# Optimization experiments

Measured on AMD Instinct MI355X. Metric: run time of the kernel, lower is better.

## Reference

```python
import jax, jax.numpy as jnp
import numpy as np

HIDDEN = 1024
N_HEADS = 16
HEAD_DIM = HIDDEN // N_HEADS


def apply_rope(x, freqs):
    # x: [b, s, h, d]; freqs: [s, d//2]
    b, s, h, d = x.shape
    x2 = x.reshape(b, s, h, d // 2, 2)
    x_real, x_imag = x2[..., 0], x2[..., 1]
    cos = jnp.cos(freqs)[None, :, None, :]  # [1, s, 1, d//2]
    sin = jnp.sin(freqs)[None, :, None, :]
    out_real = x_real * cos - x_imag * sin
    out_imag = x_real * sin + x_imag * cos
    return jnp.stack([out_real, out_imag], axis=-1).reshape(b, s, h, d)


def setup_inputs() -> dict:
    key = jax.random.key(0)
    k_x, k_f, k_wq, k_bq, k_wo, k_bo = jax.random.split(key, 6)
    b, s = 2, 2048
    x = jax.random.normal(k_x, (b, s, HIDDEN), dtype=jnp.float32)
    freqs = jax.random.normal(k_f, (s, HEAD_DIM // 2), dtype=jnp.float32)
    lim = 1.0 / np.sqrt(HIDDEN)
    W_qkv = jax.random.uniform(k_wq, (HIDDEN, 3 * HIDDEN), jnp.float32, -lim, lim)
    b_qkv = jax.random.uniform(k_bq, (3 * HIDDEN,), jnp.float32, -lim, lim)
    W_out = jax.random.uniform(k_wo, (HIDDEN, HIDDEN), jnp.float32, -lim, lim)
    b_out = jax.random.uniform(k_bo, (HIDDEN,), jnp.float32, -lim, lim)
    return {"x": x, "freqs": freqs, "W_qkv": W_qkv, "b_qkv": b_qkv,
            "W_out": W_out, "b_out": b_out}


def reference(x, freqs, W_qkv, b_qkv, W_out, b_out):
    b, s, c = x.shape
    h, d = N_HEADS, HEAD_DIM
    qkv = jnp.einsum('bsc,cf->bsf', x, W_qkv) + b_qkv  # [b, s, 3*c]
    qkv = qkv.reshape(b, s, 3, h, d)
    q, k, v = qkv[:, :, 0], qkv[:, :, 1], qkv[:, :, 2]  # [b, s, h, d]
    q = apply_rope(q, freqs)
    k = apply_rope(k, freqs)
    scale = 1.0 / np.sqrt(d).astype(np.float32)
    scores = jnp.einsum('bqhd,bkhd->bhqk', q, k) * scale  # [b, h, s, s]
    attn = jax.nn.softmax(scores, axis=-1)
    out = jnp.einsum('bhqk,bkhd->bqhd', attn, v).reshape(b, s, c)
    return jnp.einsum('bsc,cf->bsf', out, W_out) + b_out
```

## Files before the change

### kernel.cpp

```cpp
#include <hip/hip_runtime.h>
#include <math.h>

constexpr int kB = 2;
constexpr int kS = 2048;
constexpr int kC = 1024;
constexpr int kH = 16;
constexpr int kD = 64;
constexpr int kF = 3072;
constexpr int kT = kB * kS;

typedef __attribute__((ext_vector_type(8))) short short8v;
typedef __attribute__((ext_vector_type(4))) short short4v;
typedef __attribute__((ext_vector_type(4))) float f32x4;
typedef __attribute__((ext_vector_type(16))) float f32x16;

__device__ __forceinline__ short f2bf(float f) {
    unsigned u = __builtin_bit_cast(unsigned, f);
    u += 0x7fffu + ((u >> 16) & 1u);
    return (short)(u >> 16);
}

__device__ __forceinline__ unsigned cvtpk(float a, float b) {
    unsigned r;
    asm("v_cvt_pk_bf16_f32 %0, %1, %2" : "=v"(r) : "v"(a), "v"(b));
    return r;
}

__device__ __forceinline__ unsigned pk_bf16(float a, float b) {
    unsigned ua = __builtin_bit_cast(unsigned, a);
    ua += 0x7fffu + ((ua >> 16) & 1u);
    unsigned ub = __builtin_bit_cast(unsigned, b);
    ub += 0x7fffu + ((ub >> 16) & 1u);
    return (ua >> 16) | (ub & 0xffff0000u);
}

__device__ __forceinline__ void gl_lds16(const void* g, void* l) {
    __builtin_amdgcn_global_load_lds(
        (const __attribute__((address_space(1))) char*)g,
        (__attribute__((address_space(3))) char*)l, 16, 0, 0);
}

__device__ __forceinline__ f32x4 mfma16(short8v a, short8v b, f32x4 c) {
    return __builtin_amdgcn_mfma_f32_16x16x32_bf16(a, b, c, 0, 0, 0);
}
__device__ __forceinline__ f32x16 mfma32(short8v a, short8v b, f32x16 c) {
    return __builtin_amdgcn_mfma_f32_32x32x16_bf16(a, b, c, 0, 0, 0);
}

__device__ __forceinline__ void tcvt_body(const float* __restrict__ w,
                                          short* __restrict__ wt, int K, int N,
                                          int bx, int by, int t, float Ts[64][65]) {
    const int n0 = bx * 64, k0 = by * 64;
    const int r = t >> 4, c4 = (t & 15) * 4;
#pragma unroll
    for (int rr = 0; rr < 64; rr += 16) {
        float4 v = *reinterpret_cast<const float4*>(&w[(size_t)(k0 + r + rr) * N + n0 + c4]);
        Ts[r + rr][c4 + 0] = v.x; Ts[r + rr][c4 + 1] = v.y;
        Ts[r + rr][c4 + 2] = v.z; Ts[r + rr][c4 + 3] = v.w;
    }
    __syncthreads();
#pragma unroll
    for (int rr = 0; rr < 64; rr += 16) {
        int n = r + rr;
        short4v o = { f2bf(Ts[c4 + 0][n]), f2bf(Ts[c4 + 1][n]),
                      f2bf(Ts[c4 + 2][n]), f2bf(Ts[c4 + 3][n]) };
        *reinterpret_cast<short4v*>(&wt[(size_t)(n0 + n) * K + k0 + c4]) = o;
    }
}

__global__ __launch_bounds__(256) void prep_kernel(
    const float* __restrict__ x, short* __restrict__ xb,
    const float* __restrict__ wq, short* __restrict__ wqt,
    const float* __restrict__ wo, short* __restrict__ wot,
    const float* __restrict__ freqs, float* __restrict__ cost,
    float* __restrict__ sint) {
    __shared__ float Ts[64][65];
    const int bid = blockIdx.x, t = threadIdx.x;
    if (bid < 4096) {
        int i = bid * 256 + t;
        float4 v = reinterpret_cast<const float4*>(x)[i];
        short4v o = { f2bf(v.x), f2bf(v.y), f2bf(v.z), f2bf(v.w) };
        reinterpret_cast<short4v*>(xb)[i] = o;
    } else if (bid < 4864) {
        int i = bid - 4096;
        tcvt_body(wq, wqt, kC, kF, i % 48, i / 48, t, Ts);
    } else if (bid < 5120) {
        int i = bid - 4864;
        tcvt_body(wo, wot, kC, kC, i % 16, i / 16, t, Ts);
    } else {
        int i = (bid - 5120) * 256 + t;
        float f = freqs[i];
        float s, c;
        sincosf(f, &s, &c);
        cost[i] = c; sint[i] = s;
    }
}

__device__ __forceinline__ void gemm_main(const short* __restrict__ A,
                                          const short* __restrict__ Bt,
                                          int m0, int n0, short* Als, short* Bls,
                                          f32x4 acc[4][4]) {
    const int tid = threadIdx.x, wid = tid >> 6, lane = tid & 63;
    const int srow = lane >> 3, schunk = lane & 7;
    const int fr = lane & 15, fg = lane >> 4;
    const int wm = (wid >> 1) * 64, wn = (wid & 1) * 64;
    for (int kt = 0; kt < 1024; kt += 64) {
        __syncthreads();
#pragma unroll
        for (int j = 0; j < 4; ++j) {
            int i = wid * 4 + j;
            int row = i * 8 + srow;
            gl_lds16(&A[(size_t)(m0 + row) * 1024 + kt + ((schunk ^ (row & 7)) << 3)],
                     &Als[i * 512]);
        }
#pragma unroll
        for (int j = 0; j < 4; ++j) {
            int i = wid * 4 + j;
            int row = i * 8 + srow;
            gl_lds16(&Bt[(size_t)(n0 + row) * 1024 + kt + ((schunk ^ (row & 7)) << 3)],
                     &Bls[i * 512]);
        }
        __syncthreads();
#pragma unroll
        for (int kk = 0; kk < 2; ++kk) {
            short8v af[4], bf[4];
#pragma unroll
            for (int fm = 0; fm < 4; ++fm) {
                int row = wm + fm * 16 + fr;
                af[fm] = *reinterpret_cast<const short8v*>(
                    &Als[row * 64 + (((fg + 4 * kk) ^ (row & 7)) << 3)]);
            }
#pragma unroll
            for (int fn = 0; fn < 4; ++fn) {
                int row = wn + fn * 16 + fr;
                bf[fn] = *reinterpret_cast<const short8v*>(
                    &Bls[row * 64 + (((fg + 4 * kk) ^ (row & 7)) << 3)]);
            }
#pragma unroll
            for (int fm = 0; fm < 4; ++fm)
#pragma unroll
                for (int fn = 0; fn < 4; ++fn)
                    acc[fm][fn] = mfma16(af[fm], bf[fn], acc[fm][fn]);
        }
    }
}

__global__ __launch_bounds__(256) void qkv_gemm_kernel(
    const short* __restrict__ xb, const short* __restrict__ wqt,
    const float* __restrict__ bias, const float* __restrict__ cost,
    const float* __restrict__ sint,
    short* __restrict__ qg, short* __restrict__ kg, short* __restrict__ vt) {
    __shared__ __attribute__((aligned(16))) short Als[128 * 64];
    __shared__ __attribute__((aligned(16))) short Bls[128 * 64];
    f32x4 acc[4][4] = {};
    const int tid = threadIdx.x, wid = tid >> 6, lane = tid & 63;
    const int m0 = blockIdx.y * 128, n0 = blockIdx.x * 128;
    gemm_main(xb, wqt, m0, n0, Als, Bls, acc);

    const int fr = lane & 15, fg = lane >> 4;
    const int wm = (wid >> 1) * 64, wn = (wid & 1) * 64;
    const int which = (n0 + wn) >> 10;
    const int bidx = m0 >> 11;
#pragma unroll
    for (int fn = 0; fn < 4; ++fn) {
        int col = n0 + wn + fn * 16 + fr;
        float bv = bias[col];
        int d = col & 63;
        int h = (col >> 6) & 15;
        int p0 = d >> 1;
        int odd = d & 1;
#pragma unroll
        for (int fm = 0; fm < 4; ++fm) {
            int r0 = m0 + wm + fm * 16 + fg * 4;
            int s0 = r0 & 2047;
            float c[4];
#pragma unroll
            for (int r = 0; r < 4; ++r) c[r] = acc[fm][fn][r] + bv;
            if (which < 2) {
#pragma unroll
                for (int r = 0; r < 4; ++r) {
                    float cs = cost[(s0 + r) * 32 + p0];
                    float sn = sint[(s0 + r) * 32 + p0];
                    float p = __shfl_xor(c[r], 1);
                    float o = odd ? fmaf(p, sn, c[r] * cs) : fmaf(-p, sn, c[r] * cs);
                    c[r] = (which == 0) ? o * 0.1803368801f : o;
                }
                short* dst = which ? kg : qg;
                size_t base = ((size_t)(bidx * 16 + h) * 2048 + s0) * 64 + d;
#pragma unroll
                for (int r = 0; r < 4; ++r) dst[base + (size_t)r * 64] = f2bf(c[r]);
            } else {
                short4v o = { f2bf(c[0]), f2bf(c[1]), f2bf(c[2]), f2bf(c[3]) };
                *reinterpret_cast<short4v*>(
                    &vt[((size_t)(bidx * 16 + h) * 64 + d) * 2048 + s0]) = o;
            }
        }
    }
}

__global__ __launch_bounds__(256, 4) void attn_mfma_kernel(
    const short* __restrict__ qg, const short* __restrict__ kg,
    const short* __restrict__ vt, short* __restrict__ ab) {
    __shared__ __attribute__((aligned(16))) short LDSBUF[16384];
    const int tid = threadIdx.x, wid = tid >> 6, lane = tid & 63;
    const int l31 = lane & 31, hi = lane >> 5;
    const int p = wid >> 1;
    const int wq = wid & 1;
    const int r8 = lane >> 3, c8 = lane & 7;
    const int soff = 8 * (c8 ^ r8);

    const int bid = blockIdx.x;
    const int swz = (bid & 7) * 128 + (bid >> 3);
    const int bh = swz >> 5;
    const int q0 = (swz & 31) * 64 + wq * 32;

    const short* qb = qg + (size_t)bh * 2048 * 64;
    const short* kb = kg + (size_t)bh * 2048 * 64;
    const short* vb = vt + (size_t)bh * 64 * 2048;

    short8v qf[4];
#pragma unroll
    for (int kkq = 0; kkq < 4; ++kkq)
        qf[kkq] = *reinterpret_cast<const short8v*>(
            &qb[(size_t)(q0 + l31) * 64 + kkq * 16 + hi * 8]);

    f32x16 o[2] = {};
    float l_i = 0.f;

    auto stage = [&](int t, int buf) {
        const int kt = t * 32;
        short* Kd = LDSBUF + buf * 8192 + p * 2048 + (wq * 8) * 64;
        const short* Ks = kb + (size_t)(p * 1024 + kt) * 64;
#pragma unroll
        for (int j = 0; j < 2; ++j) {
            int row = j * 16 + wq * 8 + r8;
            gl_lds16(Ks + (size_t)row * 64 + soff, Kd + j * 1024);
        }
        short* Vd = LDSBUF + buf * 8192 + 4096 + (wid * 8) * 64;
        const int s = c8 ^ r8;
#pragma unroll
        for (int j = 0; j < 2; ++j) {
            int d = j * 32 + wid * 8 + r8;
            gl_lds16(vb + (size_t)d * 2048 + (s >> 2) * 1024 + kt + (s & 3) * 8,
                     Vd + j * 2048);
        }
    };

    stage(0, 0);
    __syncthreads();

    short8v pb_prev[2];
    for (int t = 0; t <= 32; ++t) {
        const int cur = t & 1, prv = cur ^ 1;
        short8v kf[4], vf0[2], vf1[2];
        if (t < 32) {
            const short* Kb = LDSBUF + cur * 8192 + p * 2048;
#pragma unroll
            for (int kkq = 0; kkq < 4; ++kkq)
                kf[kkq] = *reinterpret_cast<const short8v*>(
                    &Kb[l31 * 64 + (((kkq * 2 + hi) ^ (l31 & 7)) << 3)]);
        }
        if (t > 0) {
            const short* Vb = LDSBUF + prv * 8192 + 4096;
#pragma unroll
            for (int kk = 0; kk < 2; ++kk) {
                vf0[kk] = *reinterpret_cast<const short8v*>(
                    &Vb[l31 * 64 + (((p * 4 + kk * 2 + hi) ^ (l31 & 7)) << 3)]);
                vf1[kk] = *reinterpret_cast<const short8v*>(
                    &Vb[(32 + l31) * 64 + (((p * 4 + kk * 2 + hi) ^ (l31 & 7)) << 3)]);
            }
        }
        __syncthreads();
        if (t + 1 < 32) stage(t + 1, prv);

        f32x16 sacc = {};
        if (t < 32) {
#pragma unroll
            for (int kkq = 0; kkq < 4; ++kkq)
                sacc = mfma32(kf[kkq], qf[kkq], sacc);
        }
        if (t > 0) {
#pragma unroll
            for (int kk = 0; kk < 2; ++kk) {
                o[0] = mfma32(vf0[kk], pb_prev[kk], o[0]);
                o[1] = mfma32(vf1[kk], pb_prev[kk], o[1]);
            }
        }
        if (t < 32) {
#pragma unroll
            for (int r = 0; r < 16; ++r) sacc[r] = __builtin_amdgcn_exp2f(sacc[r]);
            unsigned c[8];
#pragma unroll
            for (int i = 0; i < 8; ++i) c[i] = cvtpk(sacc[2 * i], sacc[2 * i + 1]);
#pragma unroll
            for (int kk = 0; kk < 2; ++kk) {
                unsigned a0 = c[kk * 4 + 0], a1 = c[kk * 4 + 1];
                unsigned a2 = c[kk * 4 + 2], a3 = c[kk * 4 + 3];
                unsigned s0x = (unsigned)__shfl_xor((int)a0, 32);
                unsigned s1x = (unsigned)__shfl_xor((int)a1, 32);
                unsigned s2x = (unsigned)__shfl_xor((int)a2, 32);
                unsigned s3x = (unsigned)__shfl_xor((int)a3, 32);
                uint4 w;
                w.x = hi ? s2x : a0;
                w.y = hi ? s3x : a1;
                w.z = hi ? a2 : s0x;
                w.w = hi ? a3 : s1x;
                pb_prev[kk] = __builtin_bit_cast(short8v, w);
            }
            float t8[8];
#pragma unroll
            for (int r = 0; r < 8; ++r) t8[r] = sacc[r] + sacc[r + 8];
            float t4[4];
#pragma unroll
            for (int r = 0; r < 4; ++r) t4[r] = t8[r] + t8[r + 4];
            float rs = (t4[0] + t4[1]) + (t4[2] + t4[3]);
            rs += __shfl_xor(rs, 32);
            l_i += rs;
        }
        __syncthreads();
    }

    float* olds = reinterpret_cast<float*>(LDSBUF + 4096);
    float* lls  = olds + 2 * 2304;
    if (p == 1) {
        float* ob = olds + wq * 2304 + lane * 36;
#pragma unroll
        for (int i = 0; i < 4; ++i) {
            f32x4 w0 = { o[0][4 * i + 0], o[0][4 * i + 1], o[0][4 * i + 2], o[0][4 * i + 3] };
            *reinterpret_cast<f32x4*>(ob + i * 4) = w0;
            f32x4 w1 = { o[1][4 * i + 0], o[1][4 * i + 1], o[1][4 * i + 2], o[1][4 * i + 3] };
            *reinterpret_cast<f32x4*>(ob + 16 + i * 4) = w1;
        }
        lls[wq * 64 + lane] = l_i;
    }
    __syncthreads();
    if (p == 0) {
        float* ob = olds + wq * 2304 + lane * 36;
#pragma unroll
        for (int i = 0; i < 4; ++i) {
            f32x4 w0 = *reinterpret_cast<const f32x4*>(ob + i * 4);
            f32x4 w1 = *reinterpret_cast<const f32x4*>(ob + 16 + i * 4);
#pragma unroll
            for (int j = 0; j < 4; ++j) {
                o[0][4 * i + j] += w0[j];
                o[1][4 * i + j] += w1[j];
            }
        }
        l_i += lls[wq * 64 + lane];

        const float inv = 1.f / l_i;
        short* ep = LDSBUF + wid * 2048;
        const int q = l31;
#pragma unroll
        for (int fd = 0; fd < 2; ++fd)
#pragma unroll
            for (int i = 0; i < 4; ++i) {
                int d0 = fd * 32 + 8 * i + 4 * hi;
                uint2 w;
                w.x = pk_bf16(o[fd][4 * i + 0] * inv, o[fd][4 * i + 1] * inv);
                w.y = pk_bf16(o[fd][4 * i + 2] * inv, o[fd][4 * i + 3] * inv);
                *reinterpret_cast<uint2*>(&ep[q * 64 + (d0 ^ (8 * (q & 3)))]) = w;
            }
        __builtin_amdgcn_s_waitcnt(0);
        const int bb = bh >> 4, hh = bh & 15;
        const int wrow = r8, wcol = c8;
#pragma unroll
        for (int j = 0; j < 4; ++j) {
            int row = j * 8 + wrow;
            short8v tv = *reinterpret_cast<const short8v*>(
                &ep[row * 64 + ((8 * wcol) ^ (8 * (row & 3)))]);
            int s = q0 + row;
            *reinterpret_cast<short8v*>(
                &ab[(size_t)(bb * 2048 + s) * 1024 + hh * 64 + 8 * wcol]) = tv;
        }
    }
}

__global__ __launch_bounds__(256) void out_gemm_kernel(
    const short* __restrict__ ab, const short* __restrict__ wot,
    const float* __restrict__ bias, float* __restrict__ out) {
    __shared__ __attribute__((aligned(16))) short Als[128 * 64];
    __shared__ __attribute__((aligned(16))) short Bls[128 * 64];
    f32x4 acc[4][4] = {};
    const int tid = threadIdx.x, wid = tid >> 6, lane = tid & 63;
    const int m0 = blockIdx.y * 128, n0 = blockIdx.x * 128;
    gemm_main(ab, wot, m0, n0, Als, Bls, acc);
    const int fr = lane & 15, fg = lane >> 4;
    const int wm = (wid >> 1) * 64, wn = (wid & 1) * 64;
#pragma unroll
    for (int fn = 0; fn < 4; ++fn) {
        int col = n0 + wn + fn * 16 + fr;
        float bv = bias[col];
#pragma unroll
        for (int fm = 0; fm < 4; ++fm) {
            int r0 = m0 + wm + fm * 16 + fg * 4;
#pragma unroll
            for (int r = 0; r < 4; ++r)
                out[(size_t)(r0 + r) * 1024 + col] = acc[fm][fn][r] + bv;
        }
    }
}

extern "C" void kernel_launch(void* const* d_in, const int* in_sizes, int n_in,
                              void* d_out, int out_size, void* d_ws, size_t ws_size,
                              hipStream_t stream) {
    const float* x     = (const float*)d_in[0];
    const float* freqs = (const float*)d_in[1];
    const float* W_qkv = (const float*)d_in[2];
    const float* b_qkv = (const float*)d_in[3];
    const float* W_out = (const float*)d_in[4];
    const float* b_out = (const float*)d_in[5];
    float* out = (float*)d_out;

    char* w = (char*)d_ws;
    short* xb  = (short*)w;  w += (size_t)kT * kC * 2;
    short* wqt = (short*)w;  w += (size_t)kF * kC * 2;
    short* wot = (short*)w;  w += (size_t)kC * kC * 2;
    short* qgw = (short*)w;  w += (size_t)kB * kH * kS * kD * 2;
    short* kgw = (short*)w;  w += (size_t)kB * kH * kS * kD * 2;
    short* vtw = (short*)w;  w += (size_t)kB * kH * kS * kD * 2;
    short* abw = (short*)w;  w += (size_t)kT * kC * 2;
    float* costt = (float*)w; w += (size_t)kS * (kD / 2) * 4;
    float* sintt = (float*)w; w += (size_t)kS * (kD / 2) * 4;

    prep_kernel<<<dim3(5376), 256, 0, stream>>>(x, xb, W_qkv, wqt, W_out, wot,
                                                freqs, costt, sintt);
    qkv_gemm_kernel<<<dim3(kF / 128, kT / 128), 256, 0, stream>>>(
        xb, wqt, b_qkv, costt, sintt, qgw, kgw, vtw);
    attn_mfma_kernel<<<dim3(1024), 256, 0, stream>>>(qgw, kgw, vtw, abw);
    out_gemm_kernel<<<dim3(kC / 128, kT / 128), 256, 0, stream>>>(abw, wot, b_out, out);
}
```

Before: 133.3 us.

## Triple-buffer K/V tiles in attention with one barrier per iteration

```diff
diff --git a/kernel.cpp b/kernel.cpp
--- a/kernel.cpp
+++ b/kernel.cpp
@@ -198,10 +198,10 @@
     }
 }
 
-__global__ __launch_bounds__(256, 4) void attn_mfma_kernel(
+__global__ __launch_bounds__(256, 3) void attn_mfma_kernel(
     const short* __restrict__ qg, const short* __restrict__ kg,
     const short* __restrict__ vt, short* __restrict__ ab) {
-    __shared__ __attribute__((aligned(16))) short LDSBUF[16384];
+    __shared__ __attribute__((aligned(16))) short LDSBUF[3 * 8192];
     const int tid = threadIdx.x, wid = tid >> 6, lane = tid & 63;
     const int l31 = lane & 31, hi = lane >> 5;
     const int p = wid >> 1;
@@ -227,16 +227,16 @@
     f32x16 o[2] = {};
     float l_i = 0.f;
 
-    auto stage = [&](int t, int buf) {
+    auto stage = [&](int t, short* buf) {
         const int kt = t * 32;
-        short* Kd = LDSBUF + buf * 8192 + p * 2048 + (wq * 8) * 64;
+        short* Kd = buf + p * 2048 + (wq * 8) * 64;
         const short* Ks = kb + (size_t)(p * 1024 + kt) * 64;
 #pragma unroll
         for (int j = 0; j < 2; ++j) {
             int row = j * 16 + wq * 8 + r8;
             gl_lds16(Ks + (size_t)row * 64 + soff, Kd + j * 1024);
         }
-        short* Vd = LDSBUF + buf * 8192 + 4096 + (wid * 8) * 64;
+        short* Vd = buf + 4096 + (wid * 8) * 64;
         const int s = c8 ^ r8;
 #pragma unroll
         for (int j = 0; j < 2; ++j) {
@@ -246,79 +246,77 @@
         }
     };
 
-    stage(0, 0);
+    stage(0, LDSBUF);
+    stage(1, LDSBUF + 8192);
+
+    for (int t = 0; t < 32; ++t) {
+        __builtin_amdgcn_sched_barrier(0);
+        if (t < 31) {
+            asm volatile("s_waitcnt vmcnt(4)" ::: "memory");
+        } else {
+            asm volatile("s_waitcnt vmcnt(0)" ::: "memory");
+        }
+        __builtin_amdgcn_s_barrier();
+        __builtin_amdgcn_sched_barrier(0);
+
+        short* bufc = LDSBUF + (t % 3) * 8192;
+        if (t + 2 < 32) stage(t + 2, LDSBUF + ((t + 2) % 3) * 8192);
+
+        const short* Kb = bufc + p * 2048;
+        const short* Vb = bufc + 4096;
+
+        f32x16 sacc = {};
+#pragma unroll
+        for (int kkq = 0; kkq < 4; ++kkq) {
+            short8v a = *reinterpret_cast<const short8v*>(
+                &Kb[l31 * 64 + (((kkq * 2 + hi) ^ (l31 & 7)) << 3)]);
+            sacc = mfma32(a, qf[kkq], sacc);
+        }
+
+#pragma unroll
+        for (int r = 0; r < 16; ++r) sacc[r] = __builtin_amdgcn_exp2f(sacc[r]);
+        float t8[8];
+#pragma unroll
+        for (int r = 0; r < 8; ++r) t8[r] = sacc[r] + sacc[r + 8];
+        float t4[4];
+#pragma unroll
+        for (int r = 0; r < 4; ++r) t4[r] = t8[r] + t8[r + 4];
+        float rs = (t4[0] + t4[1]) + (t4[2] + t4[3]);
+        rs += __shfl_xor(rs, 32);
+        l_i += rs;
+
+        unsigned c[8];
+#pragma unroll
+        for (int i = 0; i < 8; ++i) c[i] = cvtpk(sacc[2 * i], sacc[2 * i + 1]);
+        short8v pb[2];
+#pragma unroll
+        for (int kk = 0; kk < 2; ++kk) {
+            unsigned a0 = c[kk * 4 + 0], a1 = c[kk * 4 + 1];
+            unsigned a2 = c[kk * 4 + 2], a3 = c[kk * 4 + 3];
+            unsigned s0x = (unsigned)__shfl_xor((int)a0, 32);
+            unsigned s1x = (unsigned)__shfl_xor((int)a1, 32);
+            unsigned s2x = (unsigned)__shfl_xor((int)a2, 32);
+            unsigned s3x = (unsigned)__shfl_xor((int)a3, 32);
+            uint4 w;
+            w.x = hi ? s2x : a0;
+            w.y = hi ? s3x : a1;
+            w.z = hi ? a2 : s0x;
+            w.w = hi ? a3 : s1x;
+            pb[kk] = __builtin_bit_cast(short8v, w);
+        }
+
+#pragma unroll
+        for (int kk = 0; kk < 2; ++kk) {
+            short8v v0 = *reinterpret_cast<const short8v*>(
+                &Vb[l31 * 64 + (((p * 4 + kk * 2 + hi) ^ (l31 & 7)) << 3)]);
+            short8v v1 = *reinterpret_cast<const short8v*>(
+                &Vb[(32 + l31) * 64 + (((p * 4 + kk * 2 + hi) ^ (l31 & 7)) << 3)]);
+            o[0] = mfma32(v0, pb[kk], o[0]);
+            o[1] = mfma32(v1, pb[kk], o[1]);
+        }
+    }
+
     __syncthreads();
-
-    short8v pb_prev[2];
-    for (int t = 0; t <= 32; ++t) {
-        const int cur = t & 1, prv = cur ^ 1;
-        short8v kf[4], vf0[2], vf1[2];
-        if (t < 32) {
-            const short* Kb = LDSBUF + cur * 8192 + p * 2048;
-#pragma unroll
-            for (int kkq = 0; kkq < 4; ++kkq)
-                kf[kkq] = *reinterpret_cast<const short8v*>(
-                    &Kb[l31 * 64 + (((kkq * 2 + hi) ^ (l31 & 7)) << 3)]);
-        }
-        if (t > 0) {
-            const short* Vb = LDSBUF + prv * 8192 + 4096;
-#pragma unroll
-            for (int kk = 0; kk < 2; ++kk) {
-                vf0[kk] = *reinterpret_cast<const short8v*>(
-                    &Vb[l31 * 64 + (((p * 4 + kk * 2 + hi) ^ (l31 & 7)) << 3)]);
-                vf1[kk] = *reinterpret_cast<const short8v*>(
-                    &Vb[(32 + l31) * 64 + (((p * 4 + kk * 2 + hi) ^ (l31 & 7)) << 3)]);
-            }
-        }
-        __syncthreads();
-        if (t + 1 < 32) stage(t + 1, prv);
-
-        f32x16 sacc = {};
-        if (t < 32) {
-#pragma unroll
-            for (int kkq = 0; kkq < 4; ++kkq)
-                sacc = mfma32(kf[kkq], qf[kkq], sacc);
-        }
-        if (t > 0) {
-#pragma unroll
-            for (int kk = 0; kk < 2; ++kk) {
-                o[0] = mfma32(vf0[kk], pb_prev[kk], o[0]);
-                o[1] = mfma32(vf1[kk], pb_prev[kk], o[1]);
-            }
-        }
-        if (t < 32) {
-#pragma unroll
-            for (int r = 0; r < 16; ++r) sacc[r] = __builtin_amdgcn_exp2f(sacc[r]);
-            unsigned c[8];
-#pragma unroll
-            for (int i = 0; i < 8; ++i) c[i] = cvtpk(sacc[2 * i], sacc[2 * i + 1]);
-#pragma unroll
-            for (int kk = 0; kk < 2; ++kk) {
-                unsigned a0 = c[kk * 4 + 0], a1 = c[kk * 4 + 1];
-                unsigned a2 = c[kk * 4 + 2], a3 = c[kk * 4 + 3];
-                unsigned s0x = (unsigned)__shfl_xor((int)a0, 32);
-                unsigned s1x = (unsigned)__shfl_xor((int)a1, 32);
-                unsigned s2x = (unsigned)__shfl_xor((int)a2, 32);
-                unsigned s3x = (unsigned)__shfl_xor((int)a3, 32);
-                uint4 w;
-                w.x = hi ? s2x : a0;
-                w.y = hi ? s3x : a1;
-                w.z = hi ? a2 : s0x;
-                w.w = hi ? a3 : s1x;
-                pb_prev[kk] = __builtin_bit_cast(short8v, w);
-            }
-            float t8[8];
-#pragma unroll
-            for (int r = 0; r < 8; ++r) t8[r] = sacc[r] + sacc[r + 8];
-            float t4[4];
-#pragma unroll
-            for (int r = 0; r < 4; ++r) t4[r] = t8[r] + t8[r + 4];
-            float rs = (t4[0] + t4[1]) + (t4[2] + t4[3]);
-            rs += __shfl_xor(rs, 32);
-            l_i += rs;
-        }
-        __syncthreads();
-    }
 
     float* olds = reinterpret_cast<float*>(LDSBUF + 4096);
     float* lls  = olds + 2 * 2304;
```

New measurement: 137.0 us. 1.03x slower.
